# Performance work log

Measured on AMD Instinct MI355X. Metric: run time of the kernel, lower is better.

## Reference

```python
import jax, jax.numpy as jnp
import numpy as np

N_WIRES = 4
N_LAYERS = 2
PATCHES = 196  # 14x14 grid of 2x2 patches


def _bexp(a, nd):
    # broadcast angle to rank nd by appending singleton axes
    a = jnp.asarray(a)
    return a.reshape(a.shape + (1,) * (nd - a.ndim))


def _apply_ry(state, wire, angle):
    # state: [B, P, 2,2,2,2]; angle broadcastable to [B, P] or scalar
    st = jnp.moveaxis(state, 2 + wire, -1)
    c = _bexp(jnp.cos(angle * 0.5), st.ndim - 1)
    s = _bexp(jnp.sin(angle * 0.5), st.ndim - 1)
    s0, s1 = st[..., 0], st[..., 1]
    out = jnp.stack([c * s0 - s * s1, s * s0 + c * s1], axis=-1)
    return jnp.moveaxis(out, -1, 2 + wire)


def _apply_cnot(state, control, target):
    st = jnp.moveaxis(state, (2 + control, 2 + target), (-2, -1))
    st = jnp.stack([st[..., 0, :], st[..., 1, ::-1]], axis=-2)
    return jnp.moveaxis(st, (-2, -1), (2 + control, 2 + target))


def _measure_z(state):
    # PauliZ expectation on each wire: sum probs * (+1/-1)
    p = state * state  # real state => |amp|^2
    outs = []
    for w in range(N_WIRES):
        axes = tuple(a for a in range(2, 2 + N_WIRES) if a != 2 + w)
        m = p.sum(axis=axes)  # [B, P, 2]
        outs.append(m[..., 0] - m[..., 1])
    return jnp.stack(outs, axis=-1)  # [B, P, 4]


def _quanv(x, theta):
    B = x.shape[0]
    # extract 2x2 patches: order (r,c),(r,c+1),(r+1,c),(r+1,c+1)
    img = x.reshape(B, 14, 2, 14, 2).transpose(0, 1, 3, 2, 4).reshape(B, PATCHES, 4)
    state = jnp.zeros((B, PATCHES, 16), x.dtype).at[:, :, 0].set(1.0)
    state = state.reshape(B, PATCHES, 2, 2, 2, 2)
    # encoder: RY(x_i) on wire i
    for w in range(N_WIRES):
        state = _apply_ry(state, w, img[:, :, w])
    # variational layers: trainable RY per wire + CNOT ring
    for l in range(N_LAYERS):
        for w in range(N_WIRES):
            state = _apply_ry(state, w, theta[l, w])
        for w in range(N_WIRES):
            state = _apply_cnot(state, w, (w + 1) % N_WIRES)
    return _measure_z(state).reshape(B, PATCHES * N_WIRES)  # [B, 784]


def setup_inputs() -> dict:
    key = jax.random.key(0)
    k = jax.random.split(key, 6)
    B = 4096
    return {
        "x": jax.random.uniform(k[0], (B, 784), jnp.float32),
        "theta": jax.random.normal(k[1], (N_LAYERS, N_WIRES), jnp.float32),
        "W1": jax.random.normal(k[2], (784, 128), jnp.float32) * 0.05,
        "b1": jnp.zeros((128,), jnp.float32),
        "W2": jax.random.normal(k[3], (128, 10), jnp.float32) * 0.05,
        "b2": jnp.zeros((10,), jnp.float32),
    }


def reference(x, theta, W1, b1, W2, b2):
    feats = _quanv(x, theta)                 # [B, 784]
    h = jax.nn.relu(feats @ W1 + b1)          # [B, 128]
    logits = h @ W2 + b2                      # [B, 10]
    return jax.nn.log_softmax(logits, axis=-1)
```

## Files before the change

### kernel.cpp

```cpp
#include <hip/hip_runtime.h>
#include <math.h>

#define PATCHES 196
#define KPAD 800
#define MROWS 16

typedef short short8 __attribute__((ext_vector_type(8)));
typedef float f32x4 __attribute__((ext_vector_type(4)));

__device__ __forceinline__ unsigned short f2bf(float f) {
  union { float f; unsigned u; } x; x.f = f;
  unsigned r = x.u + 0x7fff + ((x.u >> 16) & 1);
  return (unsigned short)(r >> 16);
}

__global__ __launch_bounds__(256) void w1t_kernel(
    const float* __restrict__ W1, unsigned short* __restrict__ w1t) {
  int idx = blockIdx.x * 256 + threadIdx.x;
  if (idx >= 128 * KPAD) return;
  int n = idx / KPAD;
  int k = idx - n * KPAD;
  float v = (k < 784) ? W1[k * 128 + n] : 0.f;
  w1t[idx] = f2bf(v);
}

__device__ __forceinline__ void apply_ry(float st[16], int bit, float c, float s) {
#pragma unroll
  for (int i = 0; i < 16; ++i) {
    if (!(i & bit)) {
      int j = i | bit;
      float a0 = st[i], a1 = st[j];
      st[i] = c * a0 - s * a1;
      st[j] = s * a0 + c * a1;
    }
  }
}

__device__ __forceinline__ void apply_cnot(float st[16], int cb, int tb) {
#pragma unroll
  for (int i = 0; i < 16; ++i) {
    if ((i & cb) && !(i & tb)) {
      int j = i | tb;
      float t = st[i]; st[i] = st[j]; st[j] = t;
    }
  }
}

__global__ __launch_bounds__(256) void quanv_kernel(
    const float* __restrict__ x, const float* __restrict__ theta,
    unsigned short* __restrict__ feats, int total) {
  __shared__ float tc[8], ts[8];
  if (threadIdx.x < 8) {
    float a = 0.5f * theta[threadIdx.x];
    tc[threadIdx.x] = __cosf(a);
    ts[threadIdx.x] = __sinf(a);
  }
  __syncthreads();

  int gid = blockIdx.x * 256 + threadIdx.x;
  if (gid >= total) return;

  int b = gid / PATCHES;
  int p = gid - b * PATCHES;
  int pr = p / 14;
  int pc = p - pr * 14;

  const float* xb = x + (size_t)b * 784 + pr * 56 + pc * 2;
  float v0 = xb[0], v1 = xb[1], v2 = xb[28], v3 = xb[29];

  float st[16];
#pragma unroll
  for (int i = 0; i < 16; ++i) st[i] = 0.f;
  st[0] = 1.f;

  apply_ry(st, 8, __cosf(0.5f * v0), __sinf(0.5f * v0));
  apply_ry(st, 4, __cosf(0.5f * v1), __sinf(0.5f * v1));
  apply_ry(st, 2, __cosf(0.5f * v2), __sinf(0.5f * v2));
  apply_ry(st, 1, __cosf(0.5f * v3), __sinf(0.5f * v3));

#pragma unroll
  for (int l = 0; l < 2; ++l) {
    apply_ry(st, 8, tc[l * 4 + 0], ts[l * 4 + 0]);
    apply_ry(st, 4, tc[l * 4 + 1], ts[l * 4 + 1]);
    apply_ry(st, 2, tc[l * 4 + 2], ts[l * 4 + 2]);
    apply_ry(st, 1, tc[l * 4 + 3], ts[l * 4 + 3]);
    apply_cnot(st, 8, 4);
    apply_cnot(st, 4, 2);
    apply_cnot(st, 2, 1);
    apply_cnot(st, 1, 8);
  }

  float m0 = 0.f, m1 = 0.f, m2 = 0.f, m3 = 0.f;
#pragma unroll
  for (int i = 0; i < 16; ++i) {
    float p2 = st[i] * st[i];
    m0 += (i & 8) ? -p2 : p2;
    m1 += (i & 4) ? -p2 : p2;
    m2 += (i & 2) ? -p2 : p2;
    m3 += (i & 1) ? -p2 : p2;
  }

  ushort4 out;
  out.x = f2bf(m0); out.y = f2bf(m1); out.z = f2bf(m2); out.w = f2bf(m3);
  *reinterpret_cast<ushort4*>(feats + (size_t)b * KPAD + p * 4) = out;

  if (p < 4) {
    ushort4 z; z.x = z.y = z.z = z.w = 0;
    *reinterpret_cast<ushort4*>(feats + (size_t)b * KPAD + 784 + p * 4) = z;
  }
}

__global__ __launch_bounds__(256) void gemm_kernel(
    const unsigned short* __restrict__ feats, const unsigned short* __restrict__ w1t,
    const float* __restrict__ b1, const float* __restrict__ W2,
    const float* __restrict__ b2, float* __restrict__ out) {
  __shared__ float hs[MROWS * 132];
  __shared__ float ls[MROWS * 10];

  const int tid = threadIdx.x;
  const int lane = tid & 63;
  const int wave = tid >> 6;
  const int m = lane & 15;
  const int quad = lane >> 4;
  const int row0 = blockIdx.x * MROWS;

  const unsigned short* ap = feats + (size_t)(row0 + m) * KPAD + quad * 8;
  const unsigned short* bp0 = w1t + (size_t)((wave * 2 + 0) * 16 + m) * KPAD + quad * 8;
  const unsigned short* bp1 = w1t + (size_t)((wave * 2 + 1) * 16 + m) * KPAD + quad * 8;

  f32x4 acc0 = {0.f, 0.f, 0.f, 0.f};
  f32x4 acc1 = {0.f, 0.f, 0.f, 0.f};

#pragma unroll 5
  for (int k0 = 0; k0 < KPAD; k0 += 32) {
    short8 a  = *reinterpret_cast<const short8*>(ap + k0);
    short8 b0 = *reinterpret_cast<const short8*>(bp0 + k0);
    short8 b1f = *reinterpret_cast<const short8*>(bp1 + k0);
    acc0 = __builtin_amdgcn_mfma_f32_16x16x32_bf16(a, b0, acc0, 0, 0, 0);
    acc1 = __builtin_amdgcn_mfma_f32_16x16x32_bf16(a, b1f, acc1, 0, 0, 0);
  }

  {
    const int col0 = (wave * 2 + 0) * 16 + m;
    const int col1 = (wave * 2 + 1) * 16 + m;
    const float bc0 = b1[col0];
    const float bc1 = b1[col1];
#pragma unroll
    for (int r = 0; r < 4; ++r) {
      const int row = quad * 4 + r;
      hs[row * 132 + col0] = fmaxf(acc0[r] + bc0, 0.f);
      hs[row * 132 + col1] = fmaxf(acc1[r] + bc1, 0.f);
    }
  }
  __syncthreads();

  if (tid < MROWS * 10) {
    const int r = tid / 10;
    const int k = tid - r * 10;
    float a = b2[k];
    const float* hr = hs + r * 132;
#pragma unroll 8
    for (int jj = 0; jj < 128; ++jj) a = fmaf(hr[jj], W2[jj * 10 + k], a);
    ls[tid] = a;
  }
  __syncthreads();

  if (tid < MROWS) {
    const int r = tid;
    float mx = ls[r * 10];
#pragma unroll
    for (int k = 1; k < 10; ++k) mx = fmaxf(mx, ls[r * 10 + k]);
    float sum = 0.f;
#pragma unroll
    for (int k = 0; k < 10; ++k) sum += expf(ls[r * 10 + k] - mx);
    const float lse = mx + logf(sum);
    float* orow = out + (size_t)(row0 + r) * 10;
#pragma unroll
    for (int k = 0; k < 10; ++k) orow[k] = ls[r * 10 + k] - lse;
  }
}

extern "C" void kernel_launch(void* const* d_in, const int* in_sizes, int n_in,
                              void* d_out, int out_size, void* d_ws, size_t ws_size,
                              hipStream_t stream) {
  const float* x     = (const float*)d_in[0];
  const float* theta = (const float*)d_in[1];
  const float* W1    = (const float*)d_in[2];
  const float* b1    = (const float*)d_in[3];
  const float* W2    = (const float*)d_in[4];
  const float* b2    = (const float*)d_in[5];
  float* out = (float*)d_out;

  const int B = in_sizes[0] / 784;

  unsigned short* feats = (unsigned short*)d_ws;
  unsigned short* w1t   = feats + (size_t)B * KPAD;

  w1t_kernel<<<(128 * KPAD + 255) / 256, 256, 0, stream>>>(W1, w1t);
  const int total = B * PATCHES;
  quanv_kernel<<<(total + 255) / 256, 256, 0, stream>>>(x, theta, feats, total);
  gemm_kernel<<<B / MROWS, 256, 0, stream>>>(feats, w1t, b1, W2, b2, out);
}
```

Before: 95.84 us.

## Fuse quanv circuit simulation into GEMM kernel with LDS fragment layout

```diff
diff --git a/kernel.cpp b/kernel.cpp
--- a/kernel.cpp
+++ b/kernel.cpp
@@ -4,6 +4,8 @@
 #define PATCHES 196
 #define KPAD 800
 #define MROWS 16
+#define CIRC (MROWS * PATCHES)
+#define FRAG_ELEMS (25 * 64 * 8)
 
 typedef short short8 __attribute__((ext_vector_type(8)));
 typedef float f32x4 __attribute__((ext_vector_type(4)));
@@ -14,14 +16,19 @@
   return (unsigned short)(r >> 16);
 }
 
-__global__ __launch_bounds__(256) void w1t_kernel(
-    const float* __restrict__ W1, unsigned short* __restrict__ w1t) {
+
+__global__ __launch_bounds__(256) void w1t_pack_kernel(
+    const float* __restrict__ W1, unsigned short* __restrict__ w1p) {
   int idx = blockIdx.x * 256 + threadIdx.x;
   if (idx >= 128 * KPAD) return;
   int n = idx / KPAD;
   int k = idx - n * KPAD;
   float v = (k < 784) ? W1[k * 128 + n] : 0.f;
-  w1t[idx] = f2bf(v);
+  int ntile = n >> 4;
+  int ki = k >> 5;
+  int quad = (k & 31) >> 3;
+  int j = k & 7;
+  w1p[ntile * FRAG_ELEMS + (ki * 64 + quad * 16 + (n & 15)) * 8 + j] = f2bf(v);
 }
 
 __device__ __forceinline__ void apply_ry(float st[16], int bit, float c, float s) {
@@ -46,96 +53,102 @@
   }
 }
 
-__global__ __launch_bounds__(256) void quanv_kernel(
+__global__ __launch_bounds__(256) void fused_kernel(
     const float* __restrict__ x, const float* __restrict__ theta,
-    unsigned short* __restrict__ feats, int total) {
+    const unsigned short* __restrict__ w1p, const float* __restrict__ b1,
+    const float* __restrict__ W2, const float* __restrict__ b2,
+    float* __restrict__ out) {
+  __shared__ unsigned short afr[FRAG_ELEMS];
   __shared__ float tc[8], ts[8];
-  if (threadIdx.x < 8) {
-    float a = 0.5f * theta[threadIdx.x];
-    tc[threadIdx.x] = __cosf(a);
-    ts[threadIdx.x] = __sinf(a);
-  }
-  __syncthreads();
-
-  int gid = blockIdx.x * 256 + threadIdx.x;
-  if (gid >= total) return;
-
-  int b = gid / PATCHES;
-  int p = gid - b * PATCHES;
-  int pr = p / 14;
-  int pc = p - pr * 14;
-
-  const float* xb = x + (size_t)b * 784 + pr * 56 + pc * 2;
-  float v0 = xb[0], v1 = xb[1], v2 = xb[28], v3 = xb[29];
-
-  float st[16];
-#pragma unroll
-  for (int i = 0; i < 16; ++i) st[i] = 0.f;
-  st[0] = 1.f;
-
-  apply_ry(st, 8, __cosf(0.5f * v0), __sinf(0.5f * v0));
-  apply_ry(st, 4, __cosf(0.5f * v1), __sinf(0.5f * v1));
-  apply_ry(st, 2, __cosf(0.5f * v2), __sinf(0.5f * v2));
-  apply_ry(st, 1, __cosf(0.5f * v3), __sinf(0.5f * v3));
-
-#pragma unroll
-  for (int l = 0; l < 2; ++l) {
-    apply_ry(st, 8, tc[l * 4 + 0], ts[l * 4 + 0]);
-    apply_ry(st, 4, tc[l * 4 + 1], ts[l * 4 + 1]);
-    apply_ry(st, 2, tc[l * 4 + 2], ts[l * 4 + 2]);
-    apply_ry(st, 1, tc[l * 4 + 3], ts[l * 4 + 3]);
-    apply_cnot(st, 8, 4);
-    apply_cnot(st, 4, 2);
-    apply_cnot(st, 2, 1);
-    apply_cnot(st, 1, 8);
-  }
-
-  float m0 = 0.f, m1 = 0.f, m2 = 0.f, m3 = 0.f;
-#pragma unroll
-  for (int i = 0; i < 16; ++i) {
-    float p2 = st[i] * st[i];
-    m0 += (i & 8) ? -p2 : p2;
-    m1 += (i & 4) ? -p2 : p2;
-    m2 += (i & 2) ? -p2 : p2;
-    m3 += (i & 1) ? -p2 : p2;
-  }
-
-  ushort4 out;
-  out.x = f2bf(m0); out.y = f2bf(m1); out.z = f2bf(m2); out.w = f2bf(m3);
-  *reinterpret_cast<ushort4*>(feats + (size_t)b * KPAD + p * 4) = out;
-
-  if (p < 4) {
-    ushort4 z; z.x = z.y = z.z = z.w = 0;
-    *reinterpret_cast<ushort4*>(feats + (size_t)b * KPAD + 784 + p * 4) = z;
-  }
-}
-
-__global__ __launch_bounds__(256) void gemm_kernel(
-    const unsigned short* __restrict__ feats, const unsigned short* __restrict__ w1t,
-    const float* __restrict__ b1, const float* __restrict__ W2,
-    const float* __restrict__ b2, float* __restrict__ out) {
   __shared__ float hs[MROWS * 132];
   __shared__ float ls[MROWS * 10];
 
   const int tid = threadIdx.x;
+  const int row0 = blockIdx.x * MROWS;
+
+  if (tid < 8) {
+    float a = 0.5f * theta[tid];
+    tc[tid] = __cosf(a);
+    ts[tid] = __sinf(a);
+  }
+  if (tid < 64) {
+    int m = tid & 15;
+    int qs = tid >> 4;
+    int quad = 2 + (qs >> 1);
+    int j0 = (qs & 1) * 4;
+    ushort4 z; z.x = z.y = z.z = z.w = 0;
+    *reinterpret_cast<ushort4*>(afr + (24 * 64 + quad * 16 + m) * 8 + j0) = z;
+  }
+  __syncthreads();
+
+  for (int c = tid; c < CIRC; c += 256) {
+    int bl = c / PATCHES;
+    int p = c - bl * PATCHES;
+    int pr = p / 14;
+    int pc = p - pr * 14;
+
+    const float* xb = x + (size_t)(row0 + bl) * 784 + pr * 56 + pc * 2;
+    float v0 = xb[0], v1 = xb[1], v2 = xb[28], v3 = xb[29];
+
+    float st[16];
+#pragma unroll
+    for (int i = 0; i < 16; ++i) st[i] = 0.f;
+    st[0] = 1.f;
+
+    apply_ry(st, 8, __cosf(0.5f * v0), __sinf(0.5f * v0));
+    apply_ry(st, 4, __cosf(0.5f * v1), __sinf(0.5f * v1));
+    apply_ry(st, 2, __cosf(0.5f * v2), __sinf(0.5f * v2));
+    apply_ry(st, 1, __cosf(0.5f * v3), __sinf(0.5f * v3));
+
+#pragma unroll
+    for (int l = 0; l < 2; ++l) {
+      apply_ry(st, 8, tc[l * 4 + 0], ts[l * 4 + 0]);
+      apply_ry(st, 4, tc[l * 4 + 1], ts[l * 4 + 1]);
+      apply_ry(st, 2, tc[l * 4 + 2], ts[l * 4 + 2]);
+      apply_ry(st, 1, tc[l * 4 + 3], ts[l * 4 + 3]);
+      apply_cnot(st, 8, 4);
+      apply_cnot(st, 4, 2);
+      apply_cnot(st, 2, 1);
+      apply_cnot(st, 1, 8);
+    }
+
+    float m0 = 0.f, m1 = 0.f, m2 = 0.f, m3 = 0.f;
+#pragma unroll
+    for (int i = 0; i < 16; ++i) {
+      float p2 = st[i] * st[i];
+      m0 += (i & 8) ? -p2 : p2;
+      m1 += (i & 4) ? -p2 : p2;
+      m2 += (i & 2) ? -p2 : p2;
+      m3 += (i & 1) ? -p2 : p2;
+    }
+
+    int K = p * 4;
+    int ki = K >> 5;
+    int quad = (K & 31) >> 3;
+    int j0 = K & 7;
+    ushort4 o;
+    o.x = f2bf(m0); o.y = f2bf(m1); o.z = f2bf(m2); o.w = f2bf(m3);
+    *reinterpret_cast<ushort4*>(afr + (ki * 64 + quad * 16 + bl) * 8 + j0) = o;
+  }
+  __syncthreads();
+
   const int lane = tid & 63;
   const int wave = tid >> 6;
   const int m = lane & 15;
   const int quad = lane >> 4;
-  const int row0 = blockIdx.x * MROWS;
-
-  const unsigned short* ap = feats + (size_t)(row0 + m) * KPAD + quad * 8;
-  const unsigned short* bp0 = w1t + (size_t)((wave * 2 + 0) * 16 + m) * KPAD + quad * 8;
-  const unsigned short* bp1 = w1t + (size_t)((wave * 2 + 1) * 16 + m) * KPAD + quad * 8;
+
+  const unsigned short* bp0 = w1p + (size_t)(wave * 2 + 0) * FRAG_ELEMS + lane * 8;
+  const unsigned short* bp1 = w1p + (size_t)(wave * 2 + 1) * FRAG_ELEMS + lane * 8;
+  const unsigned short* apl = afr + lane * 8;
 
   f32x4 acc0 = {0.f, 0.f, 0.f, 0.f};
   f32x4 acc1 = {0.f, 0.f, 0.f, 0.f};
 
 #pragma unroll 5
-  for (int k0 = 0; k0 < KPAD; k0 += 32) {
-    short8 a  = *reinterpret_cast<const short8*>(ap + k0);
-    short8 b0 = *reinterpret_cast<const short8*>(bp0 + k0);
-    short8 b1f = *reinterpret_cast<const short8*>(bp1 + k0);
+  for (int ki = 0; ki < 25; ++ki) {
+    short8 a  = *reinterpret_cast<const short8*>(apl + ki * 512);
+    short8 b0 = *reinterpret_cast<const short8*>(bp0 + ki * 512);
+    short8 b1f = *reinterpret_cast<const short8*>(bp1 + ki * 512);
     acc0 = __builtin_amdgcn_mfma_f32_16x16x32_bf16(a, b0, acc0, 0, 0, 0);
     acc1 = __builtin_amdgcn_mfma_f32_16x16x32_bf16(a, b1f, acc1, 0, 0, 0);
   }
@@ -193,11 +206,8 @@
 
   const int B = in_sizes[0] / 784;
 
-  unsigned short* feats = (unsigned short*)d_ws;
-  unsigned short* w1t   = feats + (size_t)B * KPAD;
-
-  w1t_kernel<<<(128 * KPAD + 255) / 256, 256, 0, stream>>>(W1, w1t);
-  const int total = B * PATCHES;
-  quanv_kernel<<<(total + 255) / 256, 256, 0, stream>>>(x, theta, feats, total);
-  gemm_kernel<<<B / MROWS, 256, 0, stream>>>(feats, w1t, b1, W2, b2, out);
-}
+  unsigned short* w1p = (unsigned short*)d_ws;
+
+  w1t_pack_kernel<<<(128 * KPAD + 255) / 256, 256, 0, stream>>>(W1, w1p);
+  fused_kernel<<<B / MROWS, 256, 0, stream>>>(x, theta, w1p, b1, W2, b2, out);
+}
```

New measurement: 94.15 us. About the same (-1.8%).

## Pre-pack W1 into MFMA fragment order and use eight waves per GEMM block

Applied to the files above, without the earlier changes.

```diff
diff --git a/kernel.cpp b/kernel.cpp
--- a/kernel.cpp
+++ b/kernel.cpp
@@ -4,6 +4,7 @@
 #define PATCHES 196
 #define KPAD 800
 #define MROWS 16
+#define FRAG_ELEMS (25 * 64 * 8)
 
 typedef short short8 __attribute__((ext_vector_type(8)));
 typedef float f32x4 __attribute__((ext_vector_type(4)));
@@ -14,14 +15,17 @@
   return (unsigned short)(r >> 16);
 }
 
-__global__ __launch_bounds__(256) void w1t_kernel(
-    const float* __restrict__ W1, unsigned short* __restrict__ w1t) {
+__global__ __launch_bounds__(256) void w1t_pack_kernel(
+    const float* __restrict__ W1, unsigned short* __restrict__ w1p) {
   int idx = blockIdx.x * 256 + threadIdx.x;
   if (idx >= 128 * KPAD) return;
   int n = idx / KPAD;
   int k = idx - n * KPAD;
   float v = (k < 784) ? W1[k * 128 + n] : 0.f;
-  w1t[idx] = f2bf(v);
+  int ki = k >> 5;
+  int quad = (k & 31) >> 3;
+  int j = k & 7;
+  w1p[(n >> 4) * FRAG_ELEMS + (ki * 64 + quad * 16 + (n & 15)) * 8 + j] = f2bf(v);
 }
 
 __device__ __forceinline__ void apply_ry(float st[16], int bit, float c, float s) {
@@ -100,9 +104,9 @@
     m3 += (i & 1) ? -p2 : p2;
   }
 
-  ushort4 out;
-  out.x = f2bf(m0); out.y = f2bf(m1); out.z = f2bf(m2); out.w = f2bf(m3);
-  *reinterpret_cast<ushort4*>(feats + (size_t)b * KPAD + p * 4) = out;
+  ushort4 o;
+  o.x = f2bf(m0); o.y = f2bf(m1); o.z = f2bf(m2); o.w = f2bf(m3);
+  *reinterpret_cast<ushort4*>(feats + (size_t)b * KPAD + p * 4) = o;
 
   if (p < 4) {
     ushort4 z; z.x = z.y = z.z = z.w = 0;
@@ -110,8 +114,8 @@
   }
 }
 
-__global__ __launch_bounds__(256) void gemm_kernel(
-    const unsigned short* __restrict__ feats, const unsigned short* __restrict__ w1t,
+__global__ __launch_bounds__(512) void gemm_kernel(
+    const unsigned short* __restrict__ feats, const unsigned short* __restrict__ w1p,
     const float* __restrict__ b1, const float* __restrict__ W2,
     const float* __restrict__ b2, float* __restrict__ out) {
   __shared__ float hs[MROWS * 132];
@@ -125,32 +129,30 @@
   const int row0 = blockIdx.x * MROWS;
 
   const unsigned short* ap = feats + (size_t)(row0 + m) * KPAD + quad * 8;
-  const unsigned short* bp0 = w1t + (size_t)((wave * 2 + 0) * 16 + m) * KPAD + quad * 8;
-  const unsigned short* bp1 = w1t + (size_t)((wave * 2 + 1) * 16 + m) * KPAD + quad * 8;
-
-  f32x4 acc0 = {0.f, 0.f, 0.f, 0.f};
-  f32x4 acc1 = {0.f, 0.f, 0.f, 0.f};
-
-#pragma unroll 5
-  for (int k0 = 0; k0 < KPAD; k0 += 32) {
-    short8 a  = *reinterpret_cast<const short8*>(ap + k0);
-    short8 b0 = *reinterpret_cast<const short8*>(bp0 + k0);
-    short8 b1f = *reinterpret_cast<const short8*>(bp1 + k0);
-    acc0 = __builtin_amdgcn_mfma_f32_16x16x32_bf16(a, b0, acc0, 0, 0, 0);
-    acc1 = __builtin_amdgcn_mfma_f32_16x16x32_bf16(a, b1f, acc1, 0, 0, 0);
+  const unsigned short* bp = w1p + (size_t)wave * FRAG_ELEMS + lane * 8;
+
+  f32x4 acc = {0.f, 0.f, 0.f, 0.f};
+
+#pragma unroll
+  for (int kc = 0; kc < 5; ++kc) {
+    short8 a[5], b[5];
+#pragma unroll
+    for (int u = 0; u < 5; ++u) {
+      const int ki = kc * 5 + u;
+      a[u] = *reinterpret_cast<const short8*>(ap + ki * 32);
+      b[u] = *reinterpret_cast<const short8*>(bp + ki * 512);
+    }
+#pragma unroll
+    for (int u = 0; u < 5; ++u)
+      acc = __builtin_amdgcn_mfma_f32_16x16x32_bf16(a[u], b[u], acc, 0, 0, 0);
   }
 
   {
-    const int col0 = (wave * 2 + 0) * 16 + m;
-    const int col1 = (wave * 2 + 1) * 16 + m;
-    const float bc0 = b1[col0];
-    const float bc1 = b1[col1];
-#pragma unroll
-    for (int r = 0; r < 4; ++r) {
-      const int row = quad * 4 + r;
-      hs[row * 132 + col0] = fmaxf(acc0[r] + bc0, 0.f);
-      hs[row * 132 + col1] = fmaxf(acc1[r] + bc1, 0.f);
-    }
+    const int col = wave * 16 + m;
+    const float bc = b1[col];
+#pragma unroll
+    for (int r = 0; r < 4; ++r)
+      hs[(quad * 4 + r) * 132 + col] = fmaxf(acc[r] + bc, 0.f);
   }
   __syncthreads();
 
@@ -172,8 +174,8 @@
     for (int k = 1; k < 10; ++k) mx = fmaxf(mx, ls[r * 10 + k]);
     float sum = 0.f;
 #pragma unroll
-    for (int k = 0; k < 10; ++k) sum += expf(ls[r * 10 + k] - mx);
-    const float lse = mx + logf(sum);
+    for (int k = 0; k < 10; ++k) sum += __expf(ls[r * 10 + k] - mx);
+    const float lse = mx + __logf(sum);
     float* orow = out + (size_t)(row0 + r) * 10;
 #pragma unroll
     for (int k = 0; k < 10; ++k) orow[k] = ls[r * 10 + k] - lse;
@@ -194,10 +196,10 @@
   const int B = in_sizes[0] / 784;
 
   unsigned short* feats = (unsigned short*)d_ws;
-  unsigned short* w1t   = feats + (size_t)B * KPAD;
-
-  w1t_kernel<<<(128 * KPAD + 255) / 256, 256, 0, stream>>>(W1, w1t);
+  unsigned short* w1p   = feats + (size_t)B * KPAD;
+
+  w1t_pack_kernel<<<(128 * KPAD + 255) / 256, 256, 0, stream>>>(W1, w1p);
   const int total = B * PATCHES;
   quanv_kernel<<<(total + 255) / 256, 256, 0, stream>>>(x, theta, feats, total);
-  gemm_kernel<<<B / MROWS, 256, 0, stream>>>(feats, w1t, b1, W2, b2, out);
-}
+  gemm_kernel<<<B / MROWS, 512, 0, stream>>>(feats, w1p, b1, W2, b2, out);
+}
```

New measurement: 93.34 us. 2.6% less time.
